# Performance work log

Measured on AMD Instinct MI355X. Metric: run time of the kernel, lower is better.

## Reference

```python
import jax, jax.numpy as jnp
import numpy as np

B, N, K, C, CE, H = 2, 2048, 48, 128, 128, 128
IN = 2 * C + CE  # 384
AGG_SCALE = 30.0
LN_EPS = 1e-5


def setup_inputs() -> dict:
    key = jax.random.key(0)
    ks = jax.random.split(key, 12)
    inp = {
        "node_h": jax.random.normal(ks[0], (B, N, C), jnp.float32),
        "edge_h": jax.random.normal(ks[1], (B, N, K, CE), jnp.float32),
        "edge_index": jax.random.randint(ks[2], (B, N, K), 0, N, jnp.int64),
        # message MLP: Linear(IN,H) GELU Linear(H,H) GELU Linear(H,C)
        "W1": jax.random.normal(ks[3], (IN, H), jnp.float32) / np.sqrt(IN),
        "b1": jnp.zeros((H,), jnp.float32),
        "W2": jax.random.normal(ks[4], (H, H), jnp.float32) / np.sqrt(H),
        "b2": jnp.zeros((H,), jnp.float32),
        "W3": jax.random.normal(ks[5], (H, C), jnp.float32) / np.sqrt(H),
        "b3": jnp.zeros((C,), jnp.float32),
        "Wu": jax.random.normal(ks[6], (C, C), jnp.float32) / np.sqrt(C),
        "bu": jnp.zeros((C,), jnp.float32),
        "ln_g": jnp.ones((C,), jnp.float32),
        "ln_b": jnp.zeros((C,), jnp.float32),
    }
    return inp


def _layer_norm(x, g, b):
    mu = jnp.mean(x, axis=-1, keepdims=True)
    var = jnp.var(x, axis=-1, keepdims=True)
    return (x - mu) * jax.lax.rsqrt(var + LN_EPS) * g + b


def _gelu(x):
    return jax.nn.gelu(x, approximate=False)  # torch nn.GELU default (erf)


def reference(node_h, edge_h, edge_index, W1, b1, W2, b2, W3, b3, Wu, bu, ln_g, ln_b):
    b, n, k = edge_index.shape
    c = node_h.shape[-1]
    # gather neighbor node features: (B,N,K,C)
    node_j = jnp.take_along_axis(
        node_h, edge_index.reshape(b, n * k)[..., None], axis=1
    ).reshape(b, n, k, c)
    node_i = jnp.broadcast_to(node_h[:, :, None, :], (b, n, k, c))
    edge_packed = jnp.concatenate([node_i, node_j, edge_h], axis=-1)  # (B,N,K,IN)
    # message MLP
    h = _gelu(edge_packed @ W1 + b1)
    h = _gelu(h @ W2 + b2)
    messages = (h @ W3 + b3).sum(axis=-2) / AGG_SCALE  # (B,N,C)
    # dropout is identity in eval mode
    updated_nodes = _layer_norm(node_h + messages, ln_g, ln_b)
    node_updates = updated_nodes @ Wu + bu
    out = _layer_norm(node_h + node_updates, ln_g, ln_b)
    return out
```

## Files before the change

### kernel.cpp

```cpp
#include <hip/hip_runtime.h>
#include <hip/hip_bf16.h>
#include <math.h>

#define Bn   2
#define Nn   2048
#define Kn   48
#define Cn   128
#define G2   16

typedef short bf16x8 __attribute__((ext_vector_type(8)));
typedef float f32x4  __attribute__((ext_vector_type(4)));

#if __has_builtin(__builtin_amdgcn_cvt_pk_bf16_f32)
#define HAS_PK 1
#endif

__device__ __forceinline__ short f2bf(float f) {
  union { float f; unsigned u; } v; v.f = f;
  unsigned r = v.u + 0x7fffu + ((v.u >> 16) & 1u);
  return (short)(r >> 16);
}

__device__ __forceinline__ unsigned pk2(float a, float b) {
#ifdef HAS_PK
  auto p = __builtin_amdgcn_cvt_pk_bf16_f32(a, b);
  return __builtin_bit_cast(unsigned, p);
#else
  return (unsigned)(unsigned short)f2bf(a) | ((unsigned)(unsigned short)f2bf(b) << 16);
#endif
}

__device__ __forceinline__ float gelu_f(float x) {
  float z = x * (-2.3021991f - 0.10294200f * x * x);
  float e = __builtin_amdgcn_exp2f(z);
  return x * __builtin_amdgcn_rcpf(1.0f + e);
}

__global__ void pack_weights(const float* __restrict__ W1,
                             const float* __restrict__ W2,
                             const float* __restrict__ W3,
                             const float* __restrict__ Wu,
                             short* __restrict__ ws) {
  int tid = blockIdx.x * blockDim.x + threadIdx.x;
  if (tid >= 192 * 64) return;
  int lane = tid & 63;
  int tile = tid >> 6;
  const float* W; short* dst;
  if (tile < 32)       { W = W1;         dst = ws; }
  else if (tile < 96)  { W = W1 + 16384; dst = ws + 16384; tile -= 32; }
  else if (tile < 128) { W = W2;         dst = ws + 49152; tile -= 96; }
  else if (tile < 160) { W = W3;         dst = ws + 65536; tile -= 128; }
  else                 { W = Wu;         dst = ws + 81920; tile -= 160; }
  int kt = tile >> 3, nt = tile & 7;
  int n  = nt * 16 + (lane & 15);
  int k0 = kt * 32 + (lane >> 4) * 8;
  union { short s[8]; bf16x8 v; } u8;
#pragma unroll
  for (int j = 0; j < 8; j++) u8.s[j] = f2bf(W[(k0 + j) * 128 + n]);
  *reinterpret_cast<bf16x8*>(dst + (tile << 9) + lane * 8) = u8.v;
}

__global__ __launch_bounds__(512, 4)
void node_update_kernel(const float* __restrict__ node_h,
                        const float* __restrict__ edge_h,
                        const int*   __restrict__ edge_index,
                        const short* __restrict__ wpack,
                        const float* __restrict__ b1,
                        const float* __restrict__ b2,
                        float* __restrict__ hs_out) {
  __shared__ __align__(16) char smem[25472];
  short* Xs    = (short*)smem;
  short* H1s   = (short*)smem;
  short* nhb   = (short*)(smem + 24576);
  int*   idx_s = (int*)  (smem + 25088);

  const int tid  = threadIdx.x;
  const int n0   = blockIdx.x * 2;
  const int bb   = n0 >> 11;
  const int lane = tid & 63;
  const int wave = tid >> 6;
  const int lr   = lane & 15;
  const int lq   = lane >> 4;

  const short* W1i = wpack;
  const short* W1e = wpack + 16384;
  const short* W2p = wpack + 49152;

  bf16x8 w1i[4];
#pragma unroll
  for (int kt = 0; kt < 4; kt++)
    w1i[kt] = *reinterpret_cast<const bf16x8*>(W1i + ((kt * 8 + wave) << 9) + lane * 8);
  const int colw = wave * 16 + lr;
  const float b1v = b1[colw];
  const float b2v = b2[colw];

  if (tid < 256) {
    nhb[tid] = f2bf(node_h[(size_t)n0 * Cn + tid]);
  } else if (tid < 352) {
    idx_s[tid - 256] = edge_index[n0 * Kn + (tid - 256)];
  }
  __syncthreads();

  const int gw = tid & 15;
  const int gr = tid >> 4;

  float4 na[3], nb[3];
#pragma unroll
  for (int k = 0; k < 3; k++) {
    int r = gr + k * 32;
    const float* src = node_h + (size_t)(bb * Nn + idx_s[r]) * Cn + gw * 8;
    na[k] = *reinterpret_cast<const float4*>(src);
    nb[k] = *reinterpret_cast<const float4*>(src + 4);
  }
  __builtin_amdgcn_sched_barrier(0);

  f32x4 accY[2] = {};
#pragma unroll
  for (int kt = 0; kt < 4; kt++) {
    bf16x8 avA = {}, avB = {};
    if (lr == 0) {
      avA = *reinterpret_cast<const bf16x8*>(&nhb[kt * 32 + lq * 8]);
      avB = *reinterpret_cast<const bf16x8*>(&nhb[128 + kt * 32 + lq * 8]);
    }
    accY[0] = __builtin_amdgcn_mfma_f32_16x16x32_bf16(avA, w1i[kt], accY[0], 0, 0, 0);
    accY[1] = __builtin_amdgcn_mfma_f32_16x16x32_bf16(avB, w1i[kt], accY[1], 0, 0, 0);
  }
  const float yiA = __shfl(accY[0][0], lr) + b1v;
  const float yiB = __shfl(accY[1][0], lr) + b1v;

#pragma unroll
  for (int k = 0; k < 3; k++) {
    int r = gr + k * 32;
    uint4 p;
    p.x = pk2(na[k].x, na[k].y); p.y = pk2(na[k].z, na[k].w);
    p.z = pk2(nb[k].x, nb[k].y); p.w = pk2(nb[k].z, nb[k].w);
    *reinterpret_cast<uint4*>(&Xs[r * 128 + ((gw ^ (r & 7)) << 3)]) = p;
  }
  __syncthreads();

  bf16x8 w1a[4], w1b[4];
#pragma unroll
  for (int kt = 0; kt < 4; kt++)
    w1a[kt] = *reinterpret_cast<const bf16x8*>(W1e + ((kt * 8 + wave) << 9) + lane * 8);
#pragma unroll
  for (int kt = 0; kt < 4; kt++)
    w1b[kt] = *reinterpret_cast<const bf16x8*>(W1e + (((kt + 4) * 8 + wave) << 9) + lane * 8);
  float4 ea[3], eb[3];
#pragma unroll
  for (int k = 0; k < 3; k++) {
    int r = gr + k * 32;
    const float* src = edge_h + ((size_t)n0 * Kn + r) * Cn + gw * 8;
    ea[k] = *reinterpret_cast<const float4*>(src);
    eb[k] = *reinterpret_cast<const float4*>(src + 4);
  }
  __builtin_amdgcn_sched_barrier(0);

  f32x4 acc[6] = {};
#pragma unroll
  for (int kt = 0; kt < 4; kt++) {
    int sw = (((kt * 4 + lq) ^ (lr & 7)) << 3);
#pragma unroll
    for (int m = 0; m < 6; m++) {
      bf16x8 a = *reinterpret_cast<const bf16x8*>(&Xs[(m * 16 + lr) * 128 + sw]);
      acc[m] = __builtin_amdgcn_mfma_f32_16x16x32_bf16(a, w1a[kt], acc[m], 0, 0, 0);
    }
  }
  __syncthreads();

#pragma unroll
  for (int k = 0; k < 3; k++) {
    int r = gr + k * 32;
    uint4 p;
    p.x = pk2(ea[k].x, ea[k].y); p.y = pk2(ea[k].z, ea[k].w);
    p.z = pk2(eb[k].x, eb[k].y); p.w = pk2(eb[k].z, eb[k].w);
    *reinterpret_cast<uint4*>(&Xs[r * 128 + ((gw ^ (r & 7)) << 3)]) = p;
  }
  __syncthreads();

#pragma unroll
  for (int kt = 0; kt < 4; kt++) {
    int sw = (((kt * 4 + lq) ^ (lr & 7)) << 3);
#pragma unroll
    for (int m = 0; m < 6; m++) {
      bf16x8 a = *reinterpret_cast<const bf16x8*>(&Xs[(m * 16 + lr) * 128 + sw]);
      acc[m] = __builtin_amdgcn_mfma_f32_16x16x32_bf16(a, w1b[kt], acc[m], 0, 0, 0);
    }
  }
  __syncthreads();

  {
    int g = colw >> 3, cl = colw & 7;
#pragma unroll
    for (int mt = 0; mt < 6; mt++) {
      float yi = (mt < 3) ? yiA : yiB;
      int r0 = mt * 16 + lq * 4;
      float g0 = gelu_f(acc[mt][0] + yi);
      float g1 = gelu_f(acc[mt][1] + yi);
      float g2 = gelu_f(acc[mt][2] + yi);
      float g3 = gelu_f(acc[mt][3] + yi);
      unsigned p01 = pk2(g0, g1), p23 = pk2(g2, g3);
      H1s[(r0 + 0) * 128 + ((g ^ ((r0 + 0) & 7)) << 3) + cl] = (short)(p01 & 0xffff);
      H1s[(r0 + 1) * 128 + ((g ^ ((r0 + 1) & 7)) << 3) + cl] = (short)(p01 >> 16);
      H1s[(r0 + 2) * 128 + ((g ^ ((r0 + 2) & 7)) << 3) + cl] = (short)(p23 & 0xffff);
      H1s[(r0 + 3) * 128 + ((g ^ ((r0 + 3) & 7)) << 3) + cl] = (short)(p23 >> 16);
    }
  }
  __syncthreads();

  f32x4 acc2[6] = {};
#pragma unroll
  for (int kt = 0; kt < 4; kt++) {
    bf16x8 bf = *reinterpret_cast<const bf16x8*>(W2p + ((kt * 8 + wave) << 9) + lane * 8);
    int sw = (((kt * 4 + lq) ^ (lr & 7)) << 3);
#pragma unroll
    for (int m = 0; m < 6; m++) {
      bf16x8 a = *reinterpret_cast<const bf16x8*>(&H1s[(m * 16 + lr) * 128 + sw]);
      acc2[m] = __builtin_amdgcn_mfma_f32_16x16x32_bf16(a, bf, acc2[m], 0, 0, 0);
    }
  }
  {
    float sA = 0.f, sB = 0.f;
#pragma unroll
    for (int mt = 0; mt < 3; mt++)
#pragma unroll
      for (int r = 0; r < 4; r++) {
        sA += gelu_f(acc2[mt][r] + b2v);
        sB += gelu_f(acc2[mt + 3][r] + b2v);
      }
    sA += __shfl_xor(sA, 16);
    sA += __shfl_xor(sA, 32);
    sB += __shfl_xor(sB, 16);
    sB += __shfl_xor(sB, 32);
    if (lq == 0) {
      hs_out[(size_t)n0 * Cn + colw]       = sA;
      hs_out[(size_t)(n0 + 1) * Cn + colw] = sB;
    }
  }
}

__global__ __launch_bounds__(256, 4)
void tail_kernel(const float* __restrict__ node_h,
                 const short* __restrict__ wpack,
                 const float* __restrict__ b3,
                 const float* __restrict__ bu,
                 const float* __restrict__ ln_g,
                 const float* __restrict__ ln_b,
                 float* __restrict__ out) {
  __shared__ __align__(16) char sm2[24832];
  short* hsB = (short*)sm2;
  float* nhr = (float*)(sm2 + 4096);
  float* xs  = (float*)(sm2 + 12288);
  short* usB = (short*)(sm2 + 20736);

  const int tid  = threadIdx.x;
  const int lane = tid & 63;
  const int wave = tid >> 6;
  const int lr   = lane & 15;
  const int lq   = lane >> 4;
  const int n0   = blockIdx.x * G2;

  const short* W3p = wpack + 65536;
  const short* Wup = wpack + 81920;

  {
    int row = tid >> 4, seg = tid & 15;
    const float* p = node_h + (size_t)(n0 + row) * Cn + seg * 8;
    float4 a0 = *reinterpret_cast<const float4*>(p);
    float4 a1 = *reinterpret_cast<const float4*>(p + 4);
    *reinterpret_cast<float4*>(&nhr[row * 128 + seg * 8])     = a0;
    *reinterpret_cast<float4*>(&nhr[row * 128 + seg * 8 + 4]) = a1;
    const float* q = out + (size_t)(n0 + row) * Cn + seg * 8;
    float4 c0 = *reinterpret_cast<const float4*>(q);
    float4 c1 = *reinterpret_cast<const float4*>(q + 4);
    uint4 pk;
    pk.x = pk2(c0.x, c0.y); pk.y = pk2(c0.z, c0.w);
    pk.z = pk2(c1.x, c1.y); pk.w = pk2(c1.z, c1.w);
    *reinterpret_cast<uint4*>(&hsB[row * 128 + ((seg ^ (row & 7)) << 3)]) = pk;
  }
  __syncthreads();

  f32x4 am[2] = {};
#pragma unroll
  for (int kt = 0; kt < 4; kt++) {
    bf16x8 av = *reinterpret_cast<const bf16x8*>(&hsB[lr * 128 + (((kt * 4 + lq) ^ (lr & 7)) << 3)]);
    bf16x8 bv0 = *reinterpret_cast<const bf16x8*>(W3p + ((kt * 8 + wave * 2 + 0) << 9) + lane * 8);
    bf16x8 bv1 = *reinterpret_cast<const bf16x8*>(W3p + ((kt * 8 + wave * 2 + 1) << 9) + lane * 8);
    am[0] = __builtin_amdgcn_mfma_f32_16x16x32_bf16(av, bv0, am[0], 0, 0, 0);
    am[1] = __builtin_amdgcn_mfma_f32_16x16x32_bf16(av, bv1, am[1], 0, 0, 0);
  }
#pragma unroll
  for (int j = 0; j < 2; j++) {
    int col = (wave * 2 + j) * 16 + lr;
    float bb = 48.0f * b3[col];
#pragma unroll
    for (int r = 0; r < 4; r++) {
      int row = lq * 4 + r;
      xs[row * 132 + col] = nhr[row * 128 + col] + (am[j][r] + bb) * (1.0f / 30.0f);
    }
  }
  __syncthreads();

  const float lg1 = ln_g[lane],      lb1v = ln_b[lane];
  const float lg2 = ln_g[lane + 64], lb2v = ln_b[lane + 64];
#pragma unroll
  for (int s = 0; s < 4; s++) {
    int row = wave * 4 + s;
    float v1 = xs[row * 132 + lane];
    float v2 = xs[row * 132 + lane + 64];
    float s1 = v1 + v2, s2 = v1 * v1 + v2 * v2;
#pragma unroll
    for (int off = 32; off >= 1; off >>= 1) {
      s1 += __shfl_xor(s1, off);
      s2 += __shfl_xor(s2, off);
    }
    float mu = s1 * (1.f / 128.f);
    float var = s2 * (1.f / 128.f) - mu * mu;
    float rstd = rsqrtf(var + 1e-5f);
    unsigned u12 = pk2((v1 - mu) * rstd * lg1 + lb1v,
                       (v2 - mu) * rstd * lg2 + lb2v);
    int sw = (row & 7);
    usB[row * 128 + (((lane >> 3) ^ sw) << 3) + (lane & 7)]       = (short)(u12 & 0xffff);
    usB[row * 128 + ((((lane >> 3) + 8) ^ sw) << 3) + (lane & 7)] = (short)(u12 >> 16);
  }
  __syncthreads();

  f32x4 au[2] = {};
#pragma unroll
  for (int kt = 0; kt < 4; kt++) {
    bf16x8 av = *reinterpret_cast<const bf16x8*>(&usB[lr * 128 + (((kt * 4 + lq) ^ (lr & 7)) << 3)]);
    bf16x8 bv0 = *reinterpret_cast<const bf16x8*>(Wup + ((kt * 8 + wave * 2 + 0) << 9) + lane * 8);
    bf16x8 bv1 = *reinterpret_cast<const bf16x8*>(Wup + ((kt * 8 + wave * 2 + 1) << 9) + lane * 8);
    au[0] = __builtin_amdgcn_mfma_f32_16x16x32_bf16(av, bv0, au[0], 0, 0, 0);
    au[1] = __builtin_amdgcn_mfma_f32_16x16x32_bf16(av, bv1, au[1], 0, 0, 0);
  }
  __syncthreads();
#pragma unroll
  for (int j = 0; j < 2; j++) {
    int col = (wave * 2 + j) * 16 + lr;
    float bb = bu[col];
#pragma unroll
    for (int r = 0; r < 4; r++) {
      int row = lq * 4 + r;
      xs[row * 132 + col] = nhr[row * 128 + col] + au[j][r] + bb;
    }
  }
  __syncthreads();

#pragma unroll
  for (int s = 0; s < 4; s++) {
    int row = wave * 4 + s;
    float v1 = xs[row * 132 + lane];
    float v2 = xs[row * 132 + lane + 64];
    float s1 = v1 + v2, s2 = v1 * v1 + v2 * v2;
#pragma unroll
    for (int off = 32; off >= 1; off >>= 1) {
      s1 += __shfl_xor(s1, off);
      s2 += __shfl_xor(s2, off);
    }
    float mu = s1 * (1.f / 128.f);
    float var = s2 * (1.f / 128.f) - mu * mu;
    float rstd = rsqrtf(var + 1e-5f);
    out[(size_t)(n0 + row) * Cn + lane]      = (v1 - mu) * rstd * lg1 + lb1v;
    out[(size_t)(n0 + row) * Cn + lane + 64] = (v2 - mu) * rstd * lg2 + lb2v;
  }
}

extern "C" void kernel_launch(void* const* d_in, const int* in_sizes, int n_in,
                              void* d_out, int out_size, void* d_ws, size_t ws_size,
                              hipStream_t stream) {
  const float* node_h     = (const float*)d_in[0];
  const float* edge_h     = (const float*)d_in[1];
  const int*   edge_index = (const int*)  d_in[2];
  const float* W1 = (const float*)d_in[3];
  const float* b1 = (const float*)d_in[4];
  const float* W2 = (const float*)d_in[5];
  const float* b2 = (const float*)d_in[6];
  const float* W3 = (const float*)d_in[7];
  const float* b3 = (const float*)d_in[8];
  const float* Wu = (const float*)d_in[9];
  const float* bu = (const float*)d_in[10];
  const float* ln_g = (const float*)d_in[11];
  const float* ln_b = (const float*)d_in[12];
  float* out   = (float*)d_out;
  short* wpack = (short*)d_ws;

  pack_weights<<<48, 256, 0, stream>>>(W1, W2, W3, Wu, wpack);
  node_update_kernel<<<(Bn * Nn) / 2, 512, 0, stream>>>(
      node_h, edge_h, edge_index, wpack, b1, b2, out);
  tail_kernel<<<(Bn * Nn) / G2, 256, 0, stream>>>(
      node_h, wpack, b3, bu, ln_g, ln_b, out);
}
```

Baseline: 198.9 us.

## Separate edge LDS buffer, hoist global loads, and use lightweight LDS-only barriers

After: 194.0 us. 1.03x faster.

```diff
diff --git a/kernel.cpp b/kernel.cpp
--- a/kernel.cpp
+++ b/kernel.cpp
@@ -35,6 +35,14 @@
   float e = __builtin_amdgcn_exp2f(z);
   return x * __builtin_amdgcn_rcpf(1.0f + e);
 }
+
+#define LBAR()                                              \
+  do {                                                      \
+    __builtin_amdgcn_sched_barrier(0);                      \
+    asm volatile("s_waitcnt lgkmcnt(0)" ::: "memory");      \
+    __builtin_amdgcn_s_barrier();                           \
+    __builtin_amdgcn_sched_barrier(0);                      \
+  } while (0)
 
 __global__ void pack_weights(const float* __restrict__ W1,
                              const float* __restrict__ W2,
@@ -68,11 +76,11 @@
                         const float* __restrict__ b1,
                         const float* __restrict__ b2,
                         float* __restrict__ hs_out) {
-  __shared__ __align__(16) char smem[25472];
-  short* Xs    = (short*)smem;
-  short* H1s   = (short*)smem;
-  short* nhb   = (short*)(smem + 24576);
-  int*   idx_s = (int*)  (smem + 25088);
+  __shared__ __align__(16) char smem[49664];
+  short* Xs  = (short*)smem;
+  short* H1s = (short*)smem;
+  short* Es  = (short*)(smem + 24576);
+  short* nhb = (short*)(smem + 49152);
 
   const int tid  = threadIdx.x;
   const int n0   = blockIdx.x * 2;
@@ -81,36 +89,46 @@
   const int wave = tid >> 6;
   const int lr   = lane & 15;
   const int lq   = lane >> 4;
+  const int gw   = tid & 15;
+  const int gr   = tid >> 4;
 
   const short* W1i = wpack;
   const short* W1e = wpack + 16384;
   const short* W2p = wpack + 49152;
 
-  bf16x8 w1i[4];
+  bf16x8 w1i[4], w1a[4];
 #pragma unroll
   for (int kt = 0; kt < 4; kt++)
     w1i[kt] = *reinterpret_cast<const bf16x8*>(W1i + ((kt * 8 + wave) << 9) + lane * 8);
+#pragma unroll
+  for (int kt = 0; kt < 4; kt++)
+    w1a[kt] = *reinterpret_cast<const bf16x8*>(W1e + ((kt * 8 + wave) << 9) + lane * 8);
   const int colw = wave * 16 + lr;
   const float b1v = b1[colw];
   const float b2v = b2[colw];
-
-  if (tid < 256) {
-    nhb[tid] = f2bf(node_h[(size_t)n0 * Cn + tid]);
-  } else if (tid < 352) {
-    idx_s[tid - 256] = edge_index[n0 * Kn + (tid - 256)];
-  }
-  __syncthreads();
-
-  const int gw = tid & 15;
-  const int gr = tid >> 4;
+  int idxr[3];
+#pragma unroll
+  for (int k = 0; k < 3; k++)
+    idxr[k] = edge_index[n0 * Kn + gr + k * 32];
+  if (tid < 256) nhb[tid] = f2bf(node_h[(size_t)n0 * Cn + tid]);
+  LBAR();
 
   float4 na[3], nb[3];
+#pragma unroll
+  for (int k = 0; k < 3; k++) {
+    const float* src = node_h + ((size_t)(bb * Nn) + idxr[k]) * Cn + gw * 8;
+    na[k] = *reinterpret_cast<const float4*>(src);
+    nb[k] = *reinterpret_cast<const float4*>(src + 4);
+  }
+  __builtin_amdgcn_sched_barrier(0);
+
+  float4 ea[3], eb[3];
 #pragma unroll
   for (int k = 0; k < 3; k++) {
     int r = gr + k * 32;
-    const float* src = node_h + (size_t)(bb * Nn + idx_s[r]) * Cn + gw * 8;
-    na[k] = *reinterpret_cast<const float4*>(src);
-    nb[k] = *reinterpret_cast<const float4*>(src + 4);
+    const float* src = edge_h + ((size_t)n0 * Kn + r) * Cn + gw * 8;
+    ea[k] = *reinterpret_cast<const float4*>(src);
+    eb[k] = *reinterpret_cast<const float4*>(src + 4);
   }
   __builtin_amdgcn_sched_barrier(0);
 
@@ -136,24 +154,7 @@
     p.z = pk2(nb[k].x, nb[k].y); p.w = pk2(nb[k].z, nb[k].w);
     *reinterpret_cast<uint4*>(&Xs[r * 128 + ((gw ^ (r & 7)) << 3)]) = p;
   }
-  __syncthreads();
-
-  bf16x8 w1a[4], w1b[4];
-#pragma unroll
-  for (int kt = 0; kt < 4; kt++)
-    w1a[kt] = *reinterpret_cast<const bf16x8*>(W1e + ((kt * 8 + wave) << 9) + lane * 8);
-#pragma unroll
-  for (int kt = 0; kt < 4; kt++)
-    w1b[kt] = *reinterpret_cast<const bf16x8*>(W1e + (((kt + 4) * 8 + wave) << 9) + lane * 8);
-  float4 ea[3], eb[3];
-#pragma unroll
-  for (int k = 0; k < 3; k++) {
-    int r = gr + k * 32;
-    const float* src = edge_h + ((size_t)n0 * Kn + r) * Cn + gw * 8;
-    ea[k] = *reinterpret_cast<const float4*>(src);
-    eb[k] = *reinterpret_cast<const float4*>(src + 4);
-  }
-  __builtin_amdgcn_sched_barrier(0);
+  LBAR();
 
   f32x4 acc[6] = {};
 #pragma unroll
@@ -165,7 +166,6 @@
       acc[m] = __builtin_amdgcn_mfma_f32_16x16x32_bf16(a, w1a[kt], acc[m], 0, 0, 0);
     }
   }
-  __syncthreads();
 
 #pragma unroll
   for (int k = 0; k < 3; k++) {
@@ -173,20 +173,20 @@
     uint4 p;
     p.x = pk2(ea[k].x, ea[k].y); p.y = pk2(ea[k].z, ea[k].w);
     p.z = pk2(eb[k].x, eb[k].y); p.w = pk2(eb[k].z, eb[k].w);
-    *reinterpret_cast<uint4*>(&Xs[r * 128 + ((gw ^ (r & 7)) << 3)]) = p;
-  }
-  __syncthreads();
-
-#pragma unroll
-  for (int kt = 0; kt < 4; kt++) {
+    *reinterpret_cast<uint4*>(&Es[r * 128 + ((gw ^ (r & 7)) << 3)]) = p;
+  }
+  LBAR();
+
+#pragma unroll
+  for (int kt = 0; kt < 4; kt++) {
+    bf16x8 bf = *reinterpret_cast<const bf16x8*>(W1e + (((kt + 4) * 8 + wave) << 9) + lane * 8);
     int sw = (((kt * 4 + lq) ^ (lr & 7)) << 3);
 #pragma unroll
     for (int m = 0; m < 6; m++) {
-      bf16x8 a = *reinterpret_cast<const bf16x8*>(&Xs[(m * 16 + lr) * 128 + sw]);
-      acc[m] = __builtin_amdgcn_mfma_f32_16x16x32_bf16(a, w1b[kt], acc[m], 0, 0, 0);
-    }
-  }
-  __syncthreads();
+      bf16x8 a = *reinterpret_cast<const bf16x8*>(&Es[(m * 16 + lr) * 128 + sw]);
+      acc[m] = __builtin_amdgcn_mfma_f32_16x16x32_bf16(a, bf, acc[m], 0, 0, 0);
+    }
+  }
 
   {
     int g = colw >> 3, cl = colw & 7;
@@ -205,7 +205,7 @@
       H1s[(r0 + 3) * 128 + ((g ^ ((r0 + 3) & 7)) << 3) + cl] = (short)(p23 >> 16);
     }
   }
-  __syncthreads();
+  LBAR();
 
   f32x4 acc2[6] = {};
 #pragma unroll
```
